# Optimization experiments

Measured on AMD Instinct MI355X. Metric: run time of the kernel, lower is better.

## Reference

```python
import jax, jax.numpy as jnp
import numpy as np

B, C, H, W = 8, 96, 512, 96  # W == w_size (required by the view semantics)
EPS = 1e-5


def setup_inputs() -> dict:
    key = jax.random.key(0)
    ks = jax.random.split(key, 3)
    x = jax.random.normal(ks[0], (B, C, H, W), dtype=jnp.float32)
    bn_gamma = jnp.ones((C,), jnp.float32)
    bn_beta = jnp.zeros((C,), jnp.float32)
    bn_mean = jnp.zeros((C,), jnp.float32)   # BatchNorm running mean (eval mode)
    bn_var = jnp.ones((C,), jnp.float32)     # BatchNorm running var  (eval mode)
    qkv_w = jax.random.normal(ks[1], (3 * C, C), jnp.float32) * (1.0 / np.sqrt(C))
    qkv_b = jnp.zeros((3 * C,), jnp.float32)
    return {"x": x, "bn_gamma": bn_gamma, "bn_beta": bn_beta,
            "bn_mean": bn_mean, "bn_var": bn_var,
            "qkv_w": qkv_w, "qkv_b": qkv_b}


def reference(x, bn_gamma, bn_beta, bn_mean, bn_var, qkv_w, qkv_b):
    # BatchNorm2d (eval-mode affine normalize), fused scale/shift per channel
    inv = (bn_gamma / jnp.sqrt(bn_var + EPS))[:, None, None]
    xn = (x - bn_mean[:, None, None]) * inv + bn_beta[:, None, None]
    # 1x1 conv QKV projection: [b,c,h,w] -> [b,3c,h,w]
    qkv = jnp.einsum('bchw,oc->bohw', xn, qkv_w) + qkv_b[None, :, None, None]
    q, k, v = jnp.split(qkv, 3, axis=1)  # each [b,c,h,w]
    # per-row attention over the width axis (w == w_size)
    qp = jnp.transpose(q, (0, 2, 3, 1))  # [b,h,w,c]
    kp = jnp.transpose(k, (0, 2, 3, 1))  # [b,h,w,c]
    vp = jnp.transpose(v, (0, 2, 3, 1))  # [b,h,w,c]
    score = jnp.einsum('bhqc,bhkc->bhqk', qp, kp)  # [b,h,w,w]
    attn = jax.nn.softmax(score, axis=-1)
    xt = jnp.einsum('bhqk,bhkc->bhqc', attn, vp)   # [b,h,w,c]
    out = jnp.transpose(xt, (0, 3, 1, 2)) + x       # residual add, [b,c,h,w]
    return out
```

## Files before the change

kernel.cpp:

```cpp
#include <hip/hip_runtime.h>

#define C_ 96
#define H_ 512
#define W_ 96
#define HW_ 49152
#define CHW_ 4718592
#define PIT 104
#define REG 9984

typedef _Float16 f16x8 __attribute__((ext_vector_type(8)));
typedef _Float16 f16x4 __attribute__((ext_vector_type(4)));
typedef float    f32x4 __attribute__((ext_vector_type(4)));

__global__ void prep_kernel(const float* __restrict__ wq,
                            const float* __restrict__ gamma,
                            const float* __restrict__ beta,
                            const float* __restrict__ mean,
                            const float* __restrict__ var,
                            _Float16* __restrict__ whf,
                            float* __restrict__ inv,
                            float* __restrict__ shift)
{
    int i = blockIdx.x * 256 + threadIdx.x;
    if (i < 3 * C_ * C_) whf[i] = (_Float16)wq[i];
    if (i < C_) {
        float iv = gamma[i] * rsqrtf(var[i] + 1e-5f);
        inv[i]   = iv;
        shift[i] = beta[i] - mean[i] * iv;
    }
}

__global__ __launch_bounds__(384, 3) void attn_kernel(
    const float* __restrict__ x,
    const _Float16* __restrict__ wqkv,
    const float* __restrict__ bias,
    const float* __restrict__ bninv,
    const float* __restrict__ bnshift,
    float* __restrict__ out)
{
    __shared__ _Float16 smem[3 * REG];
    _Float16* XNV = smem;
    _Float16* QP  = smem + REG;
    _Float16* Ks  = smem + 2 * REG;

    const int tid  = threadIdx.x;
    const int ws   = tid >> 6;
    const int lane = tid & 63;
    const int q4   = lane >> 4;
    const int n16  = lane & 15;

    const int bh = blockIdx.x;
    const size_t base = (size_t)(bh >> 9) * CHW_ + (size_t)(bh & 511) * W_;
    const int w0 = 16 * ws + 4 * q4;

    f32x4 xr[6];
    #pragma unroll
    for (int t = 0; t < 6; ++t) {
        const int c = 16 * t + n16;
        xr[t] = *(const f32x4*)(x + base + (size_t)c * HW_ + w0);
        const float iv = bninv[c], sh = bnshift[c];
        #pragma unroll
        for (int r = 0; r < 4; ++r)
            XNV[(w0 + r) * PIT + c] = (_Float16)(xr[t][r] * iv + sh);
    }
    __syncthreads();

    const int obase = 48 * ws;
    f32x4 acc[3][6];
    #pragma unroll
    for (int mt = 0; mt < 3; ++mt) {
        const f32x4 bb = *(const f32x4*)(bias + obase + 16 * mt + 4 * q4);
        #pragma unroll
        for (int nt = 0; nt < 6; ++nt) acc[mt][nt] = bb;
    }
    #pragma unroll
    for (int kk = 0; kk < 3; ++kk) {
        f16x8 bfr[6];
        #pragma unroll
        for (int nt = 0; nt < 6; ++nt)
            bfr[nt] = *(const f16x8*)(XNV + (16 * nt + n16) * PIT + 32 * kk + 8 * q4);
        #pragma unroll
        for (int mt = 0; mt < 3; ++mt) {
            const f16x8 afr = *(const f16x8*)(wqkv + (obase + 16 * mt + n16) * 96 + 32 * kk + 8 * q4);
            #pragma unroll
            for (int nt = 0; nt < 6; ++nt)
                acc[mt][nt] = __builtin_amdgcn_mfma_f32_16x16x32_f16(afr, bfr[nt], acc[mt][nt], 0, 0, 0);
        }
    }
    __syncthreads();

    #pragma unroll
    for (int mt = 0; mt < 3; ++mt) {
        const int o = obase + 16 * mt + 4 * q4;
        #pragma unroll
        for (int nt = 0; nt < 6; ++nt) {
            const int w = 16 * nt + n16;
            if (obase < 96) {
                f16x4 pk;
                #pragma unroll
                for (int r = 0; r < 4; ++r) pk[r] = (_Float16)acc[mt][nt][r];
                *(f16x4*)(QP + w * PIT + o) = pk;
            } else if (obase < 192) {
                f16x4 pk;
                #pragma unroll
                for (int r = 0; r < 4; ++r) pk[r] = (_Float16)acc[mt][nt][r];
                *(f16x4*)(Ks + w * PIT + (o - 96)) = pk;
            } else {
                #pragma unroll
                for (int r = 0; r < 4; ++r)
                    XNV[(o - 192 + r) * PIT + w] = (_Float16)acc[mt][nt][r];
            }
        }
    }
    __syncthreads();

    f32x4 sacc[6];
    #pragma unroll
    for (int nt = 0; nt < 6; ++nt) sacc[nt] = f32x4{0.f, 0.f, 0.f, 0.f};
    #pragma unroll
    for (int kk = 0; kk < 3; ++kk) {
        const f16x8 qa = *(const f16x8*)(QP + (16 * ws + n16) * PIT + 32 * kk + 8 * q4);
        #pragma unroll
        for (int nt = 0; nt < 6; ++nt) {
            const f16x8 kb = *(const f16x8*)(Ks + (16 * nt + n16) * PIT + 32 * kk + 8 * q4);
            sacc[nt] = __builtin_amdgcn_mfma_f32_16x16x32_f16(qa, kb, sacc[nt], 0, 0, 0);
        }
    }

    float invl[4];
    #pragma unroll
    for (int r = 0; r < 4; ++r) {
        float m = sacc[0][r];
        #pragma unroll
        for (int nt = 1; nt < 6; ++nt) m = fmaxf(m, sacc[nt][r]);
        #pragma unroll
        for (int d = 1; d < 16; d <<= 1) m = fmaxf(m, __shfl_xor(m, d, 64));
        float s = 0.f;
        #pragma unroll
        for (int nt = 0; nt < 6; ++nt) {
            const float e = __expf(sacc[nt][r] - m);
            sacc[nt][r] = e;
            s += e;
        }
        #pragma unroll
        for (int d = 1; d < 16; d <<= 1) s += __shfl_xor(s, d, 64);
        invl[r] = 1.f / s;
    }
    #pragma unroll
    for (int nt = 0; nt < 6; ++nt) {
        #pragma unroll
        for (int r = 0; r < 4; ++r)
            QP[(16 * ws + 4 * q4 + r) * PIT + 16 * nt + n16] = (_Float16)sacc[nt][r];
    }

    f32x4 oacc[6];
    #pragma unroll
    for (int nt = 0; nt < 6; ++nt) oacc[nt] = f32x4{0.f, 0.f, 0.f, 0.f};
    #pragma unroll
    for (int kk = 0; kk < 3; ++kk) {
        const f16x8 pa = *(const f16x8*)(QP + (16 * ws + n16) * PIT + 32 * kk + 8 * q4);
        #pragma unroll
        for (int nt = 0; nt < 6; ++nt) {
            const f16x8 vb = *(const f16x8*)(XNV + (16 * nt + n16) * PIT + 32 * kk + 8 * q4);
            oacc[nt] = __builtin_amdgcn_mfma_f32_16x16x32_f16(pa, vb, oacc[nt], 0, 0, 0);
        }
    }

    #pragma unroll
    for (int nt = 0; nt < 6; ++nt) {
        const int c = 16 * nt + n16;
        f32x4 o4;
        #pragma unroll
        for (int r = 0; r < 4; ++r)
            o4[r] = oacc[nt][r] * invl[r] + xr[nt][r];
        *(f32x4*)(out + base + (size_t)c * HW_ + w0) = o4;
    }
}

extern "C" void kernel_launch(void* const* d_in, const int* in_sizes, int n_in,
                              void* d_out, int out_size, void* d_ws, size_t ws_size,
                              hipStream_t stream)
{
    const float* x     = (const float*)d_in[0];
    const float* gamma = (const float*)d_in[1];
    const float* beta  = (const float*)d_in[2];
    const float* mean  = (const float*)d_in[3];
    const float* var   = (const float*)d_in[4];
    const float* qkvw  = (const float*)d_in[5];
    const float* qkvb  = (const float*)d_in[6];
    float* out = (float*)d_out;

    _Float16* whf = (_Float16*)d_ws;
    float*  inv  = (float*)((char*)d_ws + 55296);
    float*  shf  = (float*)((char*)d_ws + 55296 + 384);

    prep_kernel<<<108, 256, 0, stream>>>(qkvw, gamma, beta, mean, var, whf, inv, shf);
    attn_kernel<<<4096, 384, 0, stream>>>(x, whf, qkvb, inv, shf, out);
}
```

Before: 339.4 us.

## Keep Q in registers via lane shuffles and shrink shared memory to two regions

Each wave now computes Q only for its own 16 width rows. It rearranges the Q accumulators into MFMA A-operand layout with cross-lane shuffles instead of staging them through a shared Q buffer. K and V are computed per wave as separate output-channel slices, with V and the softmax probabilities reusing the existing shared regions behind added barriers. Shared memory per block drops by a third, and launch bounds ask for 6 blocks per CU to raise occupancy. The trade-off is shuffle overhead and a tighter register budget that could force spills.

```diff
diff --git a/kernel.cpp b/kernel.cpp
--- a/kernel.cpp
+++ b/kernel.cpp
@@ -30,7 +30,7 @@
     }
 }
 
-__global__ __launch_bounds__(384, 3) void attn_kernel(
+__global__ __launch_bounds__(384, 6) void attn_kernel(
     const float* __restrict__ x,
     const _Float16* __restrict__ wqkv,
     const float* __restrict__ bias,
@@ -38,10 +38,9 @@
     const float* __restrict__ bnshift,
     float* __restrict__ out)
 {
-    __shared__ _Float16 smem[3 * REG];
+    __shared__ _Float16 smem[2 * REG];
     _Float16* XNV = smem;
-    _Float16* QP  = smem + REG;
-    _Float16* Ks  = smem + 2 * REG;
+    _Float16* KP  = smem + REG;
 
     const int tid  = threadIdx.x;
     const int ws   = tid >> 6;
@@ -65,65 +64,100 @@
     }
     __syncthreads();
 
-    const int obase = 48 * ws;
-    f32x4 acc[3][6];
-    #pragma unroll
-    for (int mt = 0; mt < 3; ++mt) {
-        const f32x4 bb = *(const f32x4*)(bias + obase + 16 * mt + 4 * q4);
-        #pragma unroll
-        for (int nt = 0; nt < 6; ++nt) acc[mt][nt] = bb;
-    }
+    f16x8 qf[3];
+    {
+        f32x4 accq[6];
+        #pragma unroll
+        for (int mt = 0; mt < 6; ++mt)
+            accq[mt] = *(const f32x4*)(bias + 16 * mt + 4 * q4);
+        #pragma unroll
+        for (int kk = 0; kk < 3; ++kk) {
+            const f16x8 bq = *(const f16x8*)(XNV + (16 * ws + n16) * PIT + 32 * kk + 8 * q4);
+            #pragma unroll
+            for (int mt = 0; mt < 6; ++mt) {
+                const f16x8 afr = *(const f16x8*)(wqkv + (16 * mt + n16) * 96 + 32 * kk + 8 * q4);
+                accq[mt] = __builtin_amdgcn_mfma_f32_16x16x32_f16(afr, bq, accq[mt], 0, 0, 0);
+            }
+        }
+        const int l0 = n16 + 16 * ((2 * q4) & 3);
+        const int l1 = n16 + 16 * ((2 * q4 + 1) & 3);
+        const bool hi = (q4 & 2) != 0;
+        #pragma unroll
+        for (int kp = 0; kp < 3; ++kp) {
+            const f32x4 va = accq[2 * kp];
+            const f32x4 vb = accq[2 * kp + 1];
+            f16x8 q8;
+            #pragma unroll
+            for (int j = 0; j < 4; ++j) {
+                const float a0 = __shfl(va[j], l0, 64);
+                const float b0 = __shfl(vb[j], l0, 64);
+                q8[j] = (_Float16)(hi ? b0 : a0);
+                const float a1 = __shfl(va[j], l1, 64);
+                const float b1 = __shfl(vb[j], l1, 64);
+                q8[4 + j] = (_Float16)(hi ? b1 : a1);
+            }
+            qf[kp] = q8;
+        }
+    }
+
+    {
+        f32x4 acck[6];
+        {
+            const f32x4 bb = *(const f32x4*)(bias + 96 + 16 * ws + 4 * q4);
+            #pragma unroll
+            for (int nt = 0; nt < 6; ++nt) acck[nt] = bb;
+        }
+        #pragma unroll
+        for (int kk = 0; kk < 3; ++kk) {
+            const f16x8 afr = *(const f16x8*)(wqkv + (96 + 16 * ws + n16) * 96 + 32 * kk + 8 * q4);
+            #pragma unroll
+            for (int nt = 0; nt < 6; ++nt) {
+                const f16x8 bfr = *(const f16x8*)(XNV + (16 * nt + n16) * PIT + 32 * kk + 8 * q4);
+                acck[nt] = __builtin_amdgcn_mfma_f32_16x16x32_f16(afr, bfr, acck[nt], 0, 0, 0);
+            }
+        }
+        #pragma unroll
+        for (int nt = 0; nt < 6; ++nt) {
+            f16x4 pk;
+            #pragma unroll
+            for (int r = 0; r < 4; ++r) pk[r] = (_Float16)acck[nt][r];
+            *(f16x4*)(KP + (16 * nt + n16) * PIT + 16 * ws + 4 * q4) = pk;
+        }
+    }
+
+    {
+        f32x4 accv[6];
+        {
+            const f32x4 bb = *(const f32x4*)(bias + 192 + 16 * ws + 4 * q4);
+            #pragma unroll
+            for (int nt = 0; nt < 6; ++nt) accv[nt] = bb;
+        }
+        #pragma unroll
+        for (int kk = 0; kk < 3; ++kk) {
+            const f16x8 afr = *(const f16x8*)(wqkv + (192 + 16 * ws + n16) * 96 + 32 * kk + 8 * q4);
+            #pragma unroll
+            for (int nt = 0; nt < 6; ++nt) {
+                const f16x8 bfr = *(const f16x8*)(XNV + (16 * nt + n16) * PIT + 32 * kk + 8 * q4);
+                accv[nt] = __builtin_amdgcn_mfma_f32_16x16x32_f16(afr, bfr, accv[nt], 0, 0, 0);
+            }
+        }
+        __syncthreads();
+        #pragma unroll
+        for (int nt = 0; nt < 6; ++nt)
+            #pragma unroll
+            for (int r = 0; r < 4; ++r)
+                XNV[(16 * ws + 4 * q4 + r) * PIT + 16 * nt + n16] = (_Float16)accv[nt][r];
+    }
+
+    f32x4 sacc[6];
+    #pragma unroll
+    for (int nt = 0; nt < 6; ++nt) sacc[nt] = f32x4{0.f, 0.f, 0.f, 0.f};
     #pragma unroll
     for (int kk = 0; kk < 3; ++kk) {
-        f16x8 bfr[6];
-        #pragma unroll
-        for (int nt = 0; nt < 6; ++nt)
-            bfr[nt] = *(const f16x8*)(XNV + (16 * nt + n16) * PIT + 32 * kk + 8 * q4);
-        #pragma unroll
-        for (int mt = 0; mt < 3; ++mt) {
-            const f16x8 afr = *(const f16x8*)(wqkv + (obase + 16 * mt + n16) * 96 + 32 * kk + 8 * q4);
-            #pragma unroll
-            for (int nt = 0; nt < 6; ++nt)
-                acc[mt][nt] = __builtin_amdgcn_mfma_f32_16x16x32_f16(afr, bfr[nt], acc[mt][nt], 0, 0, 0);
-        }
-    }
-    __syncthreads();
-
-    #pragma unroll
-    for (int mt = 0; mt < 3; ++mt) {
-        const int o = obase + 16 * mt + 4 * q4;
-        #pragma unroll
-        for (int nt = 0; nt < 6; ++nt) {
-            const int w = 16 * nt + n16;
-            if (obase < 96) {
-                f16x4 pk;
-                #pragma unroll
-                for (int r = 0; r < 4; ++r) pk[r] = (_Float16)acc[mt][nt][r];
-                *(f16x4*)(QP + w * PIT + o) = pk;
-            } else if (obase < 192) {
-                f16x4 pk;
-                #pragma unroll
-                for (int r = 0; r < 4; ++r) pk[r] = (_Float16)acc[mt][nt][r];
-                *(f16x4*)(Ks + w * PIT + (o - 96)) = pk;
-            } else {
-                #pragma unroll
-                for (int r = 0; r < 4; ++r)
-                    XNV[(o - 192 + r) * PIT + w] = (_Float16)acc[mt][nt][r];
-            }
-        }
-    }
-    __syncthreads();
-
-    f32x4 sacc[6];
-    #pragma unroll
-    for (int nt = 0; nt < 6; ++nt) sacc[nt] = f32x4{0.f, 0.f, 0.f, 0.f};
-    #pragma unroll
-    for (int kk = 0; kk < 3; ++kk) {
-        const f16x8 qa = *(const f16x8*)(QP + (16 * ws + n16) * PIT + 32 * kk + 8 * q4);
-        #pragma unroll
-        for (int nt = 0; nt < 6; ++nt) {
-            const f16x8 kb = *(const f16x8*)(Ks + (16 * nt + n16) * PIT + 32 * kk + 8 * q4);
-            sacc[nt] = __builtin_amdgcn_mfma_f32_16x16x32_f16(qa, kb, sacc[nt], 0, 0, 0);
+        #pragma unroll
+        for (int nt = 0; nt < 6; ++nt) {
+            const f16x8 kb = *(const f16x8*)(KP + (16 * nt + n16) * PIT + 32 * kk + 8 * q4);
+            sacc[nt] = __builtin_amdgcn_mfma_f32_16x16x32_f16(qf[kk], kb, sacc[nt], 0, 0, 0);
         }
     }
 
@@ -146,19 +180,20 @@
         for (int d = 1; d < 16; d <<= 1) s += __shfl_xor(s, d, 64);
         invl[r] = 1.f / s;
     }
-    #pragma unroll
-    for (int nt = 0; nt < 6; ++nt) {
+
+    __syncthreads();
+    #pragma unroll
+    for (int nt = 0; nt < 6; ++nt)
         #pragma unroll
         for (int r = 0; r < 4; ++r)
-            QP[(16 * ws + 4 * q4 + r) * PIT + 16 * nt + n16] = (_Float16)sacc[nt][r];
-    }
+            KP[(16 * ws + 4 * q4 + r) * PIT + 16 * nt + n16] = (_Float16)sacc[nt][r];
 
     f32x4 oacc[6];
     #pragma unroll
     for (int nt = 0; nt < 6; ++nt) oacc[nt] = f32x4{0.f, 0.f, 0.f, 0.f};
     #pragma unroll
     for (int kk = 0; kk < 3; ++kk) {
-        const f16x8 pa = *(const f16x8*)(QP + (16 * ws + n16) * PIT + 32 * kk + 8 * q4);
+        const f16x8 pa = *(const f16x8*)(KP + (16 * ws + n16) * PIT + 32 * kk + 8 * q4);
         #pragma unroll
         for (int nt = 0; nt < 6; ++nt) {
             const f16x8 vb = *(const f16x8*)(XNV + (16 * nt + n16) * PIT + 32 * kk + 8 * q4);
```

Measured after the change: 381.3 us. 12.3% more time.
